# Optimization experiments

Measured on AMD Instinct MI355X. Metric: run time of the kernel, lower is better.

The kernel has to match this reference:

```python
import jax, jax.numpy as jnp
import numpy as np

D = 512
MOMENTUM = 0.99
NEG_INF = -1.0e9


def setup_inputs() -> dict:
    key = jax.random.key(0)
    ks = jax.random.split(key, 16)
    B, Lq, Lk = 16, 1024, 1024
    s = 0.02
    inp = {
        "uncond_q": jax.random.normal(ks[0], (B, D), jnp.float32),
        "q": jax.random.normal(ks[1], (B, Lq, D), jnp.float32),
        "k": jax.random.normal(ks[2], (B, Lk, D), jnp.float32),
        "v": jax.random.normal(ks[3], (B, Lk, D), jnp.float32),
        "src_key_padding_mask": jax.random.randint(ks[4], (B, Lk), 0, 2) > 0,
        "fallback_score": jnp.zeros((1,), jnp.float32),
        # parameters (torch Linear: y = x @ W.T + b)
        "Wv": jax.random.normal(ks[5], (D, D), jnp.float32) * s,
        "bv": jnp.zeros((D,), jnp.float32),
        "Wf": jax.random.normal(ks[6], (D, D), jnp.float32) * s,
        "bf": jnp.zeros((D,), jnp.float32),
        "W1": jax.random.normal(ks[7], (D, D), jnp.float32) * s,
        "b1": jnp.zeros((D,), jnp.float32),
        "W2": jax.random.normal(ks[8], (D // 2, D), jnp.float32) * s,
        "b2": jnp.zeros((D // 2,), jnp.float32),
        "W3": jax.random.normal(ks[9], (1, D // 2), jnp.float32) * s,
        "b3": jnp.zeros((1,), jnp.float32),
    }
    return inp


def _scorer(x, W1, b1, W2, b2, W3, b3):
    h = jax.nn.relu(x @ W1.T + b1)
    h = jax.nn.relu(h @ W2.T + b2)
    return jnp.tanh(h @ W3.T + b3)


def reference(uncond_q, q, k, v, src_key_padding_mask, fallback_score,
              Wv, bv, Wf, bf, W1, b1, W2, b2, W3, b3):
    B, Lq, _ = q.shape
    v_p = v @ Wv.T + bv                                  # [B,Lk,D]
    default_values = (uncond_q @ Wf.T + bf)[:, None, :]  # [B,1,D]

    scores = jnp.einsum('bqd,bkd->bqk', q, k) / jnp.sqrt(jnp.float32(D))

    # EMA fallback-score update (training mode), detached from grads
    bmax = jax.lax.stop_gradient(scores.max())
    bmin = jax.lax.stop_gradient(scores.min())
    fb = MOMENTUM * fallback_score[0] + (1.0 - MOMENTUM) * (bmax + bmin) / 2.0

    scores = jnp.where(src_key_padding_mask[:, None, :], NEG_INF, scores)
    fb_col = jnp.broadcast_to(fb, (B, Lq, 1))
    scores = jnp.concatenate([scores, fb_col], axis=-1)   # [B,Lq,Lk+1]
    weights = jax.nn.softmax(scores, axis=-1)

    v_padded = jnp.concatenate([v_p, default_values], axis=1)  # [B,Lk+1,D]
    out = jnp.einsum('bqk,bkd->bqd', weights, v_padded)

    return (_scorer(out, W1, b1, W2, b2, W3, b3),
            _scorer(default_values, W1, b1, W2, b2, W3, b3))
```

## Files before the change

### kernel.cpp

```cpp
#include <hip/hip_runtime.h>

typedef _Float16 f16;
typedef f16  f16x8 __attribute__((ext_vector_type(8)));
typedef f16  f16x4 __attribute__((ext_vector_type(4)));
typedef __fp16 fp16x2 __attribute__((ext_vector_type(2)));
typedef float f32x4 __attribute__((ext_vector_type(4)));

__device__ __forceinline__ void gld_lds16(const f16* g, void* l) {
  __builtin_amdgcn_global_load_lds((const __attribute__((address_space(1))) void*)g,
                                   (__attribute__((address_space(3))) void*)l,
                                   16, 0, 0);
}
__device__ __forceinline__ void gld_lds16f(const float* g, void* l) {
  __builtin_amdgcn_global_load_lds((const __attribute__((address_space(1))) void*)g,
                                   (__attribute__((address_space(3))) void*)l,
                                   16, 0, 0);
}

__device__ __forceinline__ f16x8 pack8(float4 a, float4 b) {
  union { f16x8 v; fp16x2 h[4]; } u;
  u.h[0] = __builtin_amdgcn_cvt_pkrtz(a.x, a.y);
  u.h[1] = __builtin_amdgcn_cvt_pkrtz(a.z, a.w);
  u.h[2] = __builtin_amdgcn_cvt_pkrtz(b.x, b.y);
  u.h[3] = __builtin_amdgcn_cvt_pkrtz(b.z, b.w);
  return u.v;
}

enum { EPI_SCORES = 0, EPI_RELU = 2, EPI_OUT = 3, EPI_BIASR = 4 };

template<int EPI, bool XMAP>
__global__ __launch_bounds__(256)
void gemm_bt(const f16* __restrict__ A, const f16* __restrict__ B, void* __restrict__ C,
             int lda, int ldb, int ldc, int K,
             long long sA, long long sB, long long sC,
             const float* __restrict__ bias, float scale,
             float* __restrict__ mmarr, int nmm,
             const float* __restrict__ wfb, const float* __restrict__ dvv,
             int nx, int nbz)
{
  __shared__ __align__(16) f16 As[4][128][32];
  __shared__ __align__(16) f16 Bs[4][128][32];
  const int tid  = threadIdx.x;
  const int lane = tid & 63;
  const int w    = tid >> 6;
  const int wm   = w >> 1, wn = w & 1;

  const int lin = blockIdx.x;
  int bz, bj;
  if constexpr (XMAP) {
    const int xcd = lin & 7, rest = lin >> 3;
    const int grp = rest / nbz;
    bj = rest - grp * nbz;
    bz = xcd + (grp << 3);
  } else {
    bz = lin / nbz; bj = lin - bz * nbz;
  }
  const int m0 = (bj / nx) * 128, n0 = (bj % nx) * 128;
  const f16* Ab = A + (size_t)bz * sA + (size_t)m0 * lda;
  const f16* Bb = B + (size_t)bz * sB + (size_t)n0 * ldb;

  f32x4 acc[4][4] = {};
  const int nsteps = K >> 5;

#define STAGE(bufb, ks)                                                              \
  {                                                                                  \
    const int k0_ = (ks) << 5;                                                       \
    _Pragma("unroll")                                                                \
    for (int i = 0; i < 2; ++i) {                                                    \
      const int ci = i * 256 + tid;                                                  \
      const int r  = ci >> 2;                                                        \
      const int sg = (ci & 3) ^ ((r >> 1) & 3);                                      \
      gld_lds16(Ab + (size_t)r * lda + k0_ + sg * 8,                                 \
                (char*)As + (bufb) + (size_t)(i * 256 + w * 64) * 16);               \
      gld_lds16(Bb + (size_t)r * ldb + k0_ + sg * 8,                                 \
                (char*)Bs + (bufb) + (size_t)(i * 256 + w * 64) * 16);               \
    }                                                                                \
  }

  STAGE(0, 0)
  if (1 < nsteps) STAGE(8192, 1)
  if (2 < nsteps) STAGE(16384, 2)

  const int elemoff = (((lane >> 4) ^ ((lane >> 1) & 3)) << 3);

  int cur = 0;
  for (int t = 0; t < nsteps; ++t) {
    if (t + 2 < nsteps)      asm volatile("s_waitcnt vmcnt(8)" ::: "memory");
    else if (t + 1 < nsteps) asm volatile("s_waitcnt vmcnt(4)" ::: "memory");
    else                     asm volatile("s_waitcnt vmcnt(0)" ::: "memory");
    __builtin_amdgcn_s_barrier();
    __builtin_amdgcn_sched_barrier(0);
    if (t + 3 < nsteps) STAGE(((cur + 3) & 3) * 8192, t + 3)
    f16x8 af[4], bfr[4];
#pragma unroll
    for (int m = 0; m < 4; ++m)
      af[m] = *(const f16x8*)&As[cur][wm * 64 + m * 16 + (lane & 15)][elemoff];
#pragma unroll
    for (int n = 0; n < 4; ++n)
      bfr[n] = *(const f16x8*)&Bs[cur][wn * 64 + n * 16 + (lane & 15)][elemoff];
    __builtin_amdgcn_s_setprio(1);
#pragma unroll
    for (int m = 0; m < 4; ++m)
#pragma unroll
      for (int n = 0; n < 4; ++n)
        acc[m][n] = __builtin_amdgcn_mfma_f32_16x16x32_f16(af[m], bfr[n], acc[m][n], 0, 0, 0);
    __builtin_amdgcn_s_setprio(0);
    cur = (cur + 1) & 3;
  }
#undef STAGE

  const int col_l = lane & 15;
  const int row_l = (lane >> 4) << 2;

  {
    f16* Ch = (f16*)C + (size_t)bz * sC + (size_t)m0 * ldc + n0;
#pragma unroll
    for (int m = 0; m < 4; ++m)
#pragma unroll
      for (int n = 0; n < 4; ++n)
#pragma unroll
        for (int r = 0; r < 4; ++r) {
          const int rr = wm * 64 + m * 16 + row_l + r;
          const int cc = wn * 64 + n * 16 + col_l;
          float val = acc[m][n][r];
          if constexpr (EPI == EPI_RELU) { val += bias[n0 + cc]; val = fmaxf(val, 0.0f); }
          if constexpr (EPI == EPI_BIASR) val += bias[m0 + rr];
          if constexpr (EPI == EPI_OUT)
            val += wfb[bz * 1024 + m0 + rr] * dvv[bz * 512 + n0 + cc];
          Ch[(size_t)rr * ldc + cc] = (f16)val;
        }
  }
  (void)scale; (void)mmarr; (void)nmm;
}

__global__ __launch_bounds__(512, 2)
void gemm256_scores(const float* __restrict__ A, const float* __restrict__ B, f16* __restrict__ C,
                    float scale, float* __restrict__ mmarr)
{
  __shared__ __align__(16) float AsF[2][256][32];
  __shared__ __align__(16) float BsF[2][256][32];
  __shared__ float redm[8], redn[8];
  const int tid  = threadIdx.x;
  const int lane = tid & 63;
  const int w    = tid >> 6;
  const int wm   = w >> 2, wn = w & 3;
  const int lin  = blockIdx.x;
  const int xcd = lin & 7, rest = lin >> 3;
  const int bj  = rest & 15;
  const int bz  = xcd + ((rest >> 4) << 3);
  const int m0 = (bj >> 2) * 256, n0 = (bj & 3) * 256;
  const float* Ab = A + (size_t)bz * 524288 + (size_t)m0 * 512;
  const float* Bb = B + (size_t)bz * 524288 + (size_t)n0 * 512;

  f32x4 acc[8][4] = {};

#define STAGEF(bufb, ks)                                                             \
  {                                                                                  \
    const int k0_ = (ks) << 5;                                                       \
    _Pragma("unroll")                                                                \
    for (int i = 0; i < 4; ++i) {                                                    \
      const int ci = i * 512 + tid;                                                  \
      const int r  = ci >> 3;                                                        \
      const int sg = (ci & 7) ^ (((ci >> 4) & 3) << 1);                              \
      gld_lds16f(Ab + (size_t)r * 512 + k0_ + sg * 4,                                \
                 (char*)AsF + (bufb) + (size_t)ci * 16);                             \
      gld_lds16f(Bb + (size_t)r * 512 + k0_ + sg * 4,                                \
                 (char*)BsF + (bufb) + (size_t)ci * 16);                             \
    }                                                                                \
  }

  STAGEF(0, 0)
  STAGEF(32768, 1)

  const int fr = lane & 15;
  const int eo = (((lane >> 4) ^ ((lane >> 1) & 3)) << 3);

  int cur = 0;
  for (int t = 0; t < 16; ++t) {
    if (t < 15) asm volatile("s_waitcnt vmcnt(8)" ::: "memory");
    else        asm volatile("s_waitcnt vmcnt(0)" ::: "memory");
    __builtin_amdgcn_s_barrier();
    __builtin_amdgcn_sched_barrier(0);
    const float* Ac = (const float*)((const char*)AsF + cur * 32768);
    const float* Bc = (const float*)((const char*)BsF + cur * 32768);
    f16x8 af[8], bfr[4];
#pragma unroll
    for (int m = 0; m < 8; ++m) {
      const float* p = Ac + (size_t)(wm * 128 + m * 16 + fr) * 32 + eo;
      af[m] = pack8(*(const float4*)p, *(const float4*)(p + 4));
    }
#pragma unroll
    for (int n = 0; n < 4; ++n) {
      const float* p = Bc + (size_t)(wn * 64 + n * 16 + fr) * 32 + eo;
      bfr[n] = pack8(*(const float4*)p, *(const float4*)(p + 4));
    }
    __builtin_amdgcn_s_setprio(1);
#pragma unroll
    for (int m = 0; m < 8; ++m)
#pragma unroll
      for (int n = 0; n < 4; ++n)
        acc[m][n] = __builtin_amdgcn_mfma_f32_16x16x32_f16(af[m], bfr[n], acc[m][n], 0, 0, 0);
    __builtin_amdgcn_s_setprio(0);
    __builtin_amdgcn_s_barrier();
    if (t + 2 < 16) STAGEF(cur * 32768, t + 2)
    cur ^= 1;
  }
#undef STAGEF

  const int col_l = lane & 15;
  const int row_l = (lane >> 4) << 2;
  f16* Ch = C + (size_t)bz * 1048576 + (size_t)m0 * 1024 + n0;
  float lmax = -3.402823466e38f, lmin = 3.402823466e38f;
#pragma unroll
  for (int m = 0; m < 8; ++m)
#pragma unroll
    for (int n = 0; n < 4; ++n)
#pragma unroll
      for (int r = 0; r < 4; ++r) {
        float val = acc[m][n][r] * scale;
        lmax = fmaxf(lmax, val); lmin = fminf(lmin, val);
        Ch[(size_t)(wm * 128 + m * 16 + row_l + r) * 1024 + (wn * 64 + n * 16 + col_l)] = (f16)val;
      }
#pragma unroll
  for (int off = 32; off >= 1; off >>= 1) {
    lmax = fmaxf(lmax, __shfl_xor(lmax, off));
    lmin = fminf(lmin, __shfl_xor(lmin, off));
  }
  if (lane == 0) { redm[w] = lmax; redn[w] = lmin; }
  __syncthreads();
  if (tid == 0) {
    float gm = redm[0], gn = redn[0];
#pragma unroll
    for (int i = 1; i < 8; ++i) { gm = fmaxf(gm, redm[i]); gn = fminf(gn, redn[i]); }
    mmarr[lin] = gm; mmarr[256 + lin] = gn;
  }
}

__global__ __launch_bounds__(256)
void reduce_mm(const float* __restrict__ mmarr, int n,
               const float* __restrict__ fallback, float* __restrict__ fbv,
               const unsigned char* __restrict__ mask, unsigned* __restrict__ mm)
{
  __shared__ float rm[4], rn[4];
  __shared__ int redc[256];
  const int lane = threadIdx.x & 63, w = threadIdx.x >> 6;
  float mx = -3.402823466e38f, mn = 3.402823466e38f;
  for (int i = threadIdx.x; i < n; i += 256) {
    mx = fmaxf(mx, mmarr[i]);
    mn = fminf(mn, mmarr[n + i]);
  }
#pragma unroll
  for (int off = 32; off >= 1; off >>= 1) {
    mx = fmaxf(mx, __shfl_xor(mx, off));
    mn = fminf(mn, __shfl_xor(mn, off));
  }
  if (lane == 0) { rm[w] = mx; rn[w] = mn; }
  int c = 0;
  for (int i = threadIdx.x; i < 16384; i += 256) c += (mask[i] != 0) ? 1 : 0;
  redc[threadIdx.x] = c;
  __syncthreads();
  for (int s = 128; s > 0; s >>= 1) {
    if (threadIdx.x < s) redc[threadIdx.x] += redc[threadIdx.x + s];
    __syncthreads();
  }
  if (threadIdx.x == 0) {
    float gmax = fmaxf(fmaxf(rm[0], rm[1]), fmaxf(rm[2], rm[3]));
    float gmin = fminf(fminf(rn[0], rn[1]), fminf(rn[2], rn[3]));
    fbv[0] = 0.99f * fallback[0] + 0.005f * (gmax + gmin);
    mm[0] = (unsigned)redc[0];
  }
}

__global__ __launch_bounds__(256)
void front_k(const float* __restrict__ v, f16* __restrict__ v16,
             const float* __restrict__ wv, const float* __restrict__ w1,
             const float* __restrict__ w2,
             f16* __restrict__ owv, f16* __restrict__ ow1, f16* __restrict__ ow2,
             const float* __restrict__ uq, const float* __restrict__ Wf,
             const float* __restrict__ bfv, float* __restrict__ dv)
{
  const int blk = blockIdx.x;
  if (blk < 2048) {
    const int i = blk * 256 + threadIdx.x;
#pragma unroll
    for (int it = 0; it < 4; ++it) {
      const size_t j = (size_t)i + (size_t)it * 524288;
      float4 x = *(const float4*)(v + j * 4);
      f16x4 o = { (f16)x.x, (f16)x.y, (f16)x.z, (f16)x.w };
      *(f16x4*)(v16 + j * 4) = o;
    }
  } else if (blk < 2688) {
    int i = (blk - 2048) * 256 + threadIdx.x;
    const float* src; f16* dst; int j;
    if (i < 65536)       { src = wv; dst = owv; j = i; }
    else if (i < 131072) { src = w1; dst = ow1; j = i - 65536; }
    else                 { src = w2; dst = ow2; j = i - 131072; }
    float4 x = *(const float4*)(src + (size_t)j * 4);
    f16x4 o = { (f16)x.x, (f16)x.y, (f16)x.z, (f16)x.w };
    *(f16x4*)(dst + (size_t)j * 4) = o;
  } else {
    const int gw   = ((blk - 2688) * 256 + threadIdx.x) >> 6;
    const int lane = threadIdx.x & 63;
    const int b = gw >> 9, j = gw & 511;
    const float* x  = uq + (size_t)b * 512;
    const float* wr = Wf + (size_t)j * 512;
    const int o = lane * 8;
    float4 x0 = *(const float4*)(x + o),  x1 = *(const float4*)(x + o + 4);
    float4 w0 = *(const float4*)(wr + o), w1v = *(const float4*)(wr + o + 4);
    float s = x0.x*w0.x + x0.y*w0.y + x0.z*w0.z + x0.w*w0.w
            + x1.x*w1v.x + x1.y*w1v.y + x1.z*w1v.z + x1.w*w1v.w;
#pragma unroll
    for (int off = 32; off >= 1; off >>= 1) s += __shfl_xor(s, off);
    if (lane == 0) dv[gw] = s + bfv[j];
  }
}

__global__ __launch_bounds__(256)
void softmax_rows(const f16* __restrict__ scores, const void* __restrict__ maskp,
                  const float* __restrict__ fbv, const unsigned* __restrict__ mm,
                  f16* __restrict__ Wt, float* __restrict__ wfb)
{
  __shared__ float red[8];
  const int row  = blockIdx.x;
  const int b    = row >> 10;
  const int tid  = threadIdx.x;
  const int lane = tid & 63, w = tid >> 6;
  const float fb = fbv[0];
  const unsigned mode = (mm[0] > 5000u) ? 1u : 0u;
  const f16* s = scores + (size_t)row * 1024;
  const int k0 = tid * 4;
  f16x4 sv = *(const f16x4*)(s + k0);
  float x[4];
  if (mode) {
    const unsigned char* m8 = (const unsigned char*)maskp + b * 1024 + k0;
    x[0] = m8[0] ? -1e9f : (float)sv[0];  x[1] = m8[1] ? -1e9f : (float)sv[1];
    x[2] = m8[2] ? -1e9f : (float)sv[2];  x[3] = m8[3] ? -1e9f : (float)sv[3];
  } else {
    const int* mi = (const int*)maskp + b * 1024 + k0;
    x[0] = mi[0] ? -1e9f : (float)sv[0];  x[1] = mi[1] ? -1e9f : (float)sv[1];
    x[2] = mi[2] ? -1e9f : (float)sv[2];  x[3] = mi[3] ? -1e9f : (float)sv[3];
  }
  float mx = fmaxf(fmaxf(x[0], x[1]), fmaxf(x[2], x[3]));
#pragma unroll
  for (int off = 32; off >= 1; off >>= 1) mx = fmaxf(mx, __shfl_xor(mx, off));
  if (lane == 0) red[w] = mx;
  __syncthreads();
  mx = fmaxf(fmaxf(fmaxf(red[0], red[1]), fmaxf(red[2], red[3])), fb);
  float e0 = expf(x[0] - mx), e1 = expf(x[1] - mx), e2 = expf(x[2] - mx), e3 = expf(x[3] - mx);
  float sum = (e0 + e1) + (e2 + e3);
#pragma unroll
  for (int off = 32; off >= 1; off >>= 1) sum += __shfl_xor(sum, off);
  if (lane == 0) red[4 + w] = sum;
  __syncthreads();
  float efb = expf(fb - mx);
  float Z = ((red[4] + red[5]) + (red[6] + red[7])) + efb;
  float inv = 1.0f / Z;
  f16x4 o = { (f16)(e0 * inv), (f16)(e1 * inv), (f16)(e2 * inv), (f16)(e3 * inv) };
  *(f16x4*)&Wt[(size_t)row * 1024 + k0] = o;
  if (tid == 0) wfb[row] = efb * inv;
}

template<int IN, int ACT>
__global__ __launch_bounds__(256)
void fc_wave(const float* __restrict__ X, const float* __restrict__ W,
             const float* __restrict__ bias, float* __restrict__ Y, int OutN)
{
  const int gw   = (blockIdx.x * 256 + threadIdx.x) >> 6;
  const int lane = threadIdx.x & 63;
  const int b = gw / OutN, j = gw - b * OutN;
  const float* x  = X + (size_t)b * IN;
  const float* wr = W + (size_t)j * IN;
  float s = 0.f;
  if constexpr (IN == 512) {
    const int o = lane * 8;
    float4 x0 = *(const float4*)(x + o),  x1 = *(const float4*)(x + o + 4);
    float4 w0 = *(const float4*)(wr + o), w1 = *(const float4*)(wr + o + 4);
    s = x0.x*w0.x + x0.y*w0.y + x0.z*w0.z + x0.w*w0.w
      + x1.x*w1.x + x1.y*w1.y + x1.z*w1.z + x1.w*w1.w;
  } else {
    const int o = lane * 4;
    float4 x0 = *(const float4*)(x + o);
    float4 w0 = *(const float4*)(wr + o);
    s = x0.x*w0.x + x0.y*w0.y + x0.z*w0.z + x0.w*w0.w;
  }
#pragma unroll
  for (int off = 32; off >= 1; off >>= 1) s += __shfl_xor(s, off);
  if (lane == 0) {
    float val = s + bias[ACT == 2 ? 0 : j];
    if constexpr (ACT == 1) val = fmaxf(val, 0.f);
    if constexpr (ACT == 2) val = tanhf(val);
    Y[gw] = val;
  }
}

__global__ __launch_bounds__(256)
void y_kernel(const f16* __restrict__ h2, const float* __restrict__ W3,
              const float* __restrict__ b3, float* __restrict__ outp)
{
  int row = blockIdx.x * 16 + (threadIdx.x >> 4);
  int l   = threadIdx.x & 15;
  const f16* h = h2 + (size_t)row * 256 + l * 16;
  float s = 0.f;
#pragma unroll
  for (int j = 0; j < 16; ++j) s += (float)h[j] * W3[l * 16 + j];
#pragma unroll
  for (int off = 1; off < 16; off <<= 1) s += __shfl_xor(s, off);
  if (l == 0) outp[row] = tanhf(s + b3[0]);
}

extern "C" void kernel_launch(void* const* d_in, const int* in_sizes, int n_in,
                              void* d_out, int out_size, void* d_ws, size_t ws_size,
                              hipStream_t stream) {
  const float* uq       = (const float*)d_in[0];
  const float* q        = (const float*)d_in[1];
  const float* kk       = (const float*)d_in[2];
  const float* v        = (const float*)d_in[3];
  const void*  mask     = d_in[4];
  const float* fallback = (const float*)d_in[5];
  const float* Wv = (const float*)d_in[6];
  const float* bv = (const float*)d_in[7];
  const float* Wf = (const float*)d_in[8];
  const float* bf = (const float*)d_in[9];
  const float* W1 = (const float*)d_in[10];
  const float* b1 = (const float*)d_in[11];
  const float* W2 = (const float*)d_in[12];
  const float* b2 = (const float*)d_in[13];
  const float* W3 = (const float*)d_in[14];
  const float* b3 = (const float*)d_in[15];
  float* outp = (float*)d_out;

  char* ws = (char*)d_ws;
  const size_t MB = 1ull << 20;
  f16*  scores = (f16*)ws;
  f16*  h1b  = (f16*)ws;
  f16*  h2b  = (f16*)(ws + 16 * MB);
  f16*  vpt  = (f16*)(ws + 32 * MB);
  f16*  outb = (f16*)(ws + 48 * MB);
  f16*  wts  = (f16*)(ws + 64 * MB);
  f16*  v16  = (f16*)(ws + 96 * MB);
  char* cst  = ws + 112 * MB;
  f16*  Wv16 = (f16*)(cst);
  f16*  W116 = (f16*)(cst + 512 * 1024);
  f16*  W216 = (f16*)(cst + 1024 * 1024);
  float* dv   = (float*)(cst + 1280 * 1024);
  float* wfb  = (float*)(cst + 1312 * 1024);
  float* h1d  = (float*)(cst + 1376 * 1024);
  float* h2d  = (float*)(cst + 1408 * 1024);
  unsigned* mm = (unsigned*)(cst + 1424 * 1024);
  float* fbv   = (float*)(cst + 1428 * 1024);
  float* mmarr = (float*)(cst + 1432 * 1024);

  front_k<<<4736, 256, 0, stream>>>(v, v16, Wv, W1, W2, Wv16, W116, W216,
                                    uq, Wf, bf, dv);

  gemm256_scores<<<256, 512, 0, stream>>>(q, kk, scores, 0.04419417382415922f, mmarr);

  reduce_mm<<<1, 256, 0, stream>>>(mmarr, 256, fallback, fbv,
                                   (const unsigned char*)mask, mm);

  softmax_rows<<<16384, 256, 0, stream>>>(scores, mask, fbv, mm, wts, wfb);

  gemm_bt<EPI_BIASR, true><<<512, 256, 0, stream>>>(
      Wv16, v16, vpt, 512, 512, 1024, 512,
      0LL, 524288LL, 524288LL,
      bv, 1.f, nullptr, 0, nullptr, nullptr, 8, 32);

  gemm_bt<EPI_OUT, true><<<512, 256, 0, stream>>>(
      wts, vpt, outb, 1024, 1024, 512, 1024,
      1048576LL, 524288LL, 524288LL,
      nullptr, 1.f, nullptr, 0, wfb, dv, 4, 32);

  gemm_bt<EPI_RELU, false><<<512, 256, 0, stream>>>(
      outb, W116, h1b, 512, 512, 512, 512, 0LL, 0LL, 0LL,
      b1, 1.f, nullptr, 0, nullptr, nullptr, 4, 512);

  gemm_bt<EPI_RELU, false><<<256, 256, 0, stream>>>(
      h1b, W216, h2b, 512, 512, 256, 512, 0LL, 0LL, 0LL,
      b2, 1.f, nullptr, 0, nullptr, nullptr, 2, 256);

  y_kernel<<<1024, 256, 0, stream>>>(h2b, W3, b3, outp);

  fc_wave<512, 1><<<2048, 256, 0, stream>>>(dv, W1, b1, h1d, 512);
  fc_wave<512, 1><<<1024, 256, 0, stream>>>(h1d, W2, b2, h2d, 256);
  fc_wave<256, 2><<<4, 256, 0, stream>>>(h2d, W3, b3, outp + 16384, 1);

  (void)in_sizes; (void)n_in; (void)out_size; (void)ws_size;
}
```

Measured before the change: 169.7 us.

## Stage scores GEMM operands as fp16 in LDS via register loads, triple-buffered

The scores GEMM no longer copies fp32 tiles straight into LDS with async global-to-LDS loads and converts them at fragment-read time. Each thread now loads fp32 through registers, packs to fp16 once, and writes into a three-stage fp16 LDS ring. This halves LDS footprint and read traffic and removes repeated conversion in the MFMA loop, with one barrier per iteration. The cost is that global loads now pass through VGPRs, adding register pressure, and the loads may no longer overlap as well with compute.

```diff
diff --git a/kernel.cpp b/kernel.cpp
--- a/kernel.cpp
+++ b/kernel.cpp
@@ -7,11 +7,6 @@
 typedef float f32x4 __attribute__((ext_vector_type(4)));
 
 __device__ __forceinline__ void gld_lds16(const f16* g, void* l) {
-  __builtin_amdgcn_global_load_lds((const __attribute__((address_space(1))) void*)g,
-                                   (__attribute__((address_space(3))) void*)l,
-                                   16, 0, 0);
-}
-__device__ __forceinline__ void gld_lds16f(const float* g, void* l) {
   __builtin_amdgcn_global_load_lds((const __attribute__((address_space(1))) void*)g,
                                    (__attribute__((address_space(3))) void*)l,
                                    16, 0, 0);
@@ -137,8 +132,8 @@
 void gemm256_scores(const float* __restrict__ A, const float* __restrict__ B, f16* __restrict__ C,
                     float scale, float* __restrict__ mmarr)
 {
-  __shared__ __align__(16) float AsF[2][256][32];
-  __shared__ __align__(16) float BsF[2][256][32];
+  __shared__ __align__(16) f16 As[3][256][32];
+  __shared__ __align__(16) f16 Bs[3][256][32];
   __shared__ float redm[8], redn[8];
   const int tid  = threadIdx.x;
   const int lane = tid & 63;
@@ -152,48 +147,56 @@
   const float* Ab = A + (size_t)bz * 524288 + (size_t)m0 * 512;
   const float* Bb = B + (size_t)bz * 524288 + (size_t)n0 * 512;
 
+  const int r0  = tid >> 2;
+  const int sg0 = (tid & 3) ^ ((r0 >> 1) & 3);
+  const size_t offG = (size_t)r0 * 512 + sg0 * 8;
+  f16* const dstA0 = (f16*)As + (size_t)tid * 8;
+  f16* const dstB0 = (f16*)Bs + (size_t)tid * 8;
+
   f32x4 acc[8][4] = {};
 
-#define STAGEF(bufb, ks)                                                             \
-  {                                                                                  \
-    const int k0_ = (ks) << 5;                                                       \
-    _Pragma("unroll")                                                                \
-    for (int i = 0; i < 4; ++i) {                                                    \
-      const int ci = i * 512 + tid;                                                  \
-      const int r  = ci >> 3;                                                        \
-      const int sg = (ci & 7) ^ (((ci >> 4) & 3) << 1);                              \
-      gld_lds16f(Ab + (size_t)r * 512 + k0_ + sg * 4,                                \
-                 (char*)AsF + (bufb) + (size_t)ci * 16);                             \
-      gld_lds16f(Bb + (size_t)r * 512 + k0_ + sg * 4,                                \
-                 (char*)BsF + (bufb) + (size_t)ci * 16);                             \
-    }                                                                                \
-  }
-
-  STAGEF(0, 0)
-  STAGEF(32768, 1)
+#pragma unroll
+  for (int s = 0; s < 2; ++s) {
+    const int k0 = s << 5;
+    float4 a0 = *(const float4*)(Ab + offG + k0);
+    float4 a1 = *(const float4*)(Ab + offG + k0 + 4);
+    float4 a2 = *(const float4*)(Ab + offG + k0 + 65536);
+    float4 a3 = *(const float4*)(Ab + offG + k0 + 65540);
+    float4 b0 = *(const float4*)(Bb + offG + k0);
+    float4 b1 = *(const float4*)(Bb + offG + k0 + 4);
+    float4 b2 = *(const float4*)(Bb + offG + k0 + 65536);
+    float4 b3 = *(const float4*)(Bb + offG + k0 + 65540);
+    *(f16x8*)(dstA0 + s * 8192)        = pack8(a0, a1);
+    *(f16x8*)(dstA0 + s * 8192 + 4096) = pack8(a2, a3);
+    *(f16x8*)(dstB0 + s * 8192)        = pack8(b0, b1);
+    *(f16x8*)(dstB0 + s * 8192 + 4096) = pack8(b2, b3);
+  }
+  __syncthreads();
 
   const int fr = lane & 15;
-  const int eo = (((lane >> 4) ^ ((lane >> 1) & 3)) << 3);
+  const int elemoff = (((lane >> 4) ^ ((lane >> 1) & 3)) << 3);
 
   int cur = 0;
   for (int t = 0; t < 16; ++t) {
-    if (t < 15) asm volatile("s_waitcnt vmcnt(8)" ::: "memory");
-    else        asm volatile("s_waitcnt vmcnt(0)" ::: "memory");
-    __builtin_amdgcn_s_barrier();
-    __builtin_amdgcn_sched_barrier(0);
-    const float* Ac = (const float*)((const char*)AsF + cur * 32768);
-    const float* Bc = (const float*)((const char*)BsF + cur * 32768);
+    float4 a0, a1, a2, a3, b0, b1, b2, b3;
+    if (t + 2 < 16) {
+      const int k0 = (t + 2) << 5;
+      a0 = *(const float4*)(Ab + offG + k0);
+      a1 = *(const float4*)(Ab + offG + k0 + 4);
+      a2 = *(const float4*)(Ab + offG + k0 + 65536);
+      a3 = *(const float4*)(Ab + offG + k0 + 65540);
+      b0 = *(const float4*)(Bb + offG + k0);
+      b1 = *(const float4*)(Bb + offG + k0 + 4);
+      b2 = *(const float4*)(Bb + offG + k0 + 65536);
+      b3 = *(const float4*)(Bb + offG + k0 + 65540);
+    }
     f16x8 af[8], bfr[4];
 #pragma unroll
-    for (int m = 0; m < 8; ++m) {
-      const float* p = Ac + (size_t)(wm * 128 + m * 16 + fr) * 32 + eo;
-      af[m] = pack8(*(const float4*)p, *(const float4*)(p + 4));
-    }
-#pragma unroll
-    for (int n = 0; n < 4; ++n) {
-      const float* p = Bc + (size_t)(wn * 64 + n * 16 + fr) * 32 + eo;
-      bfr[n] = pack8(*(const float4*)p, *(const float4*)(p + 4));
-    }
+    for (int m = 0; m < 8; ++m)
+      af[m] = *(const f16x8*)&As[cur][wm * 128 + m * 16 + fr][elemoff];
+#pragma unroll
+    for (int n = 0; n < 4; ++n)
+      bfr[n] = *(const f16x8*)&Bs[cur][wn * 64 + n * 16 + fr][elemoff];
     __builtin_amdgcn_s_setprio(1);
 #pragma unroll
     for (int m = 0; m < 8; ++m)
@@ -201,11 +204,16 @@
       for (int n = 0; n < 4; ++n)
         acc[m][n] = __builtin_amdgcn_mfma_f32_16x16x32_f16(af[m], bfr[n], acc[m][n], 0, 0, 0);
     __builtin_amdgcn_s_setprio(0);
-    __builtin_amdgcn_s_barrier();
-    if (t + 2 < 16) STAGEF(cur * 32768, t + 2)
-    cur ^= 1;
-  }
-#undef STAGEF
+    if (t + 2 < 16) {
+      int wb = cur + 2; if (wb >= 3) wb -= 3;
+      *(f16x8*)(dstA0 + wb * 8192)        = pack8(a0, a1);
+      *(f16x8*)(dstA0 + wb * 8192 + 4096) = pack8(a2, a3);
+      *(f16x8*)(dstB0 + wb * 8192)        = pack8(b0, b1);
+      *(f16x8*)(dstB0 + wb * 8192 + 4096) = pack8(b2, b3);
+    }
+    __syncthreads();
+    cur = (cur + 1 == 3) ? 0 : cur + 1;
+  }
 
   const int col_l = lane & 15;
   const int row_l = (lane >> 4) << 2;
```

After: 161.7 us. 1.05x faster.
